# Kernel tuning notes

Measured on AMD Instinct MI355X. Metric: run time of the kernel, lower is better.

## Reference

```python
import jax, jax.numpy as jnp
import numpy as np

N = 10000        # num_nodes
F_IN = 256       # dataset_num_features
H = 128          # hidden_channels
C_OUT = 40       # dataset_num_classes
L = 3            # num_layers
HEADS = 8
DH = H // HEADS  # per-head dim
E = 160000       # num edges (before self loops)
SCALE = 1.0 / float(np.sqrt(DH))


def setup_inputs() -> dict:
    key = jax.random.key(0)
    ks = jax.random.split(key, 8)
    s = lambda k, *sh: (jax.random.normal(k, sh, dtype=jnp.float32) * 0.05)
    return dict(
        edge_index=jax.random.randint(ks[0], (2, E), 0, N, dtype=jnp.int32),
        x_param=s(ks[1], N, F_IN),
        lin1_w=s(ks[2], F_IN, H),
        lin1_b=jnp.zeros((H,), jnp.float32),
        wq=s(ks[3], L, H, H),
        wk=s(ks[4], L, H, H),
        wv=s(ks[5], L, H, H),
        bq=jnp.zeros((L, H), jnp.float32),
        bk=jnp.zeros((L, H), jnp.float32),
        bv=jnp.zeros((L, H), jnp.float32),
        lin2_w=s(ks[6], H, C_OUT),
        lin2_b=jnp.zeros((C_OUT,), jnp.float32),
    )


def _gcn_norm(edge_index):
    # PyG gcn_norm: add self loops (weight 1), symmetric D^-1/2 A D^-1/2
    loops = jnp.arange(N, dtype=edge_index.dtype)
    row = jnp.concatenate([edge_index[0], loops])  # source j
    col = jnp.concatenate([edge_index[1], loops])  # target i
    deg = jax.ops.segment_sum(jnp.ones(row.shape, jnp.float32), col, num_segments=N)
    dis = jnp.where(deg > 0, jax.lax.rsqrt(jnp.maximum(deg, 1e-12)), 0.0)
    return row, col, dis[row] * dis[col]


def _restricted_softmax(score):
    # softmax with an implicit extra logit at `margin=0`
    m = jnp.maximum(jnp.max(score, axis=-1, keepdims=True), 0.0)
    e = jnp.exp(score - m)
    return e / (jnp.sum(e, axis=-1, keepdims=True) + jnp.exp(-m))


def _forward(edge_index, x_param, lin1_w, lin1_b, wq, wk, wv, bq, bk, bv, lin2_w, lin2_b):
    row, col, norm = _gcn_norm(edge_index)
    # dropouts are eval-mode no-ops
    x = jax.nn.relu(x_param @ lin1_w + lin1_b)  # [N, H]
    x_all = x[:, None, :]                       # [N, 1, H]
    for l in range(L):
        t = x_all.shape[1]
        # project per-node first (linear commutes with per-edge gather)
        q = (x_all[:, -1] @ wq[l] + bq[l]).reshape(N, HEADS, DH)      # query from latest state
        k = (x_all @ wk[l] + bk[l]).reshape(N, t, HEADS, DH)          # keys over full history
        v = (x_all @ wv[l] + bv[l]).reshape(N, t, HEADS, DH)
        qe = q[col]   # [Etot, heads, dh]   (x_i)
        ke = k[row]   # [Etot, t, heads, dh] (x_j)
        ve = v[row]
        score = jnp.einsum('ehd,ethd->eht', qe, ke) * SCALE
        attn = _restricted_softmax(score)        # attention-dropout is a no-op in eval
        msg = jnp.einsum('eht,ethd->ehd', attn, ve).reshape(-1, H) * norm[:, None]
        out = jax.ops.segment_sum(msg, col, num_segments=N)  # aggr='add'
        x = jax.nn.relu(out)
        x_all = jnp.concatenate([x_all, x[:, None, :]], axis=1)
    logits = x_all[:, -1] @ lin2_w + lin2_b
    return jax.nn.log_softmax(logits, axis=1)


def reference(edge_index, x_param, lin1_w, lin1_b, wq, wk, wv, bq, bk, bv, lin2_w, lin2_b):
    return _forward(edge_index, x_param, lin1_w, lin1_b, wq, wk, wv, bq, bk, bv, lin2_w, lin2_b)
```

## Files before the change

### kernel.cpp

```cpp
#include <hip/hip_runtime.h>
#include <math.h>

#define N_NODES 10000
#define F_IN_D  256
#define H_DIM   128
#define C_OUTD  40
#define NHEADS  8
#define NEDGES  160000
#define ETOT    (NEDGES + N_NODES)
#define SCALE_F 0.25f
#define TILES_N 157

typedef __attribute__((ext_vector_type(8))) short bf16x8;
typedef __attribute__((ext_vector_type(4))) float f32x4;
typedef __attribute__((ext_vector_type(2))) float f32x2;

__device__ __forceinline__ unsigned short f2bf(float f) {
    unsigned int u = __float_as_uint(f);
    unsigned int r = (u + 0x7FFFu + ((u >> 16) & 1u)) >> 16;
    return (unsigned short)r;
}
__device__ __forceinline__ float bf2f(unsigned short h) {
    return __uint_as_float(((unsigned int)h) << 16);
}
__device__ __forceinline__ unsigned char f2fp8(float v) {
    int pk = __builtin_amdgcn_cvt_pk_fp8_f32(v, v, 0, false);
    return (unsigned char)(pk & 0xff);
}


__global__ void k_deg_count(const int* __restrict__ col, int* degi) {
    int e = blockIdx.x * 256 + threadIdx.x;
    if (e < NEDGES) atomicAdd(&degi[col[e]], 1);
}

__global__ void k_scan(const int* __restrict__ degi, int* offsets, int* cursor) {
    __shared__ int part[256];
    int tid = threadIdx.x;
    int s = 0;
    if (tid < 250) {
        const int4* d4 = (const int4*)degi;
        for (int i = 0; i < 10; ++i) {
            int4 v = d4[tid * 10 + i];
            s += v.x + v.y + v.z + v.w;
        }
    }
    part[tid] = s;
    __syncthreads();
    for (int off = 1; off < 256; off <<= 1) {
        int v = 0;
        if (tid >= off) v = part[tid - off];
        __syncthreads();
        part[tid] += v;
        __syncthreads();
    }
    if (tid < 250) {
        int base = part[tid] - s;
        int beg = tid * 40;
        for (int i = 0; i < 40; ++i) {
            offsets[beg + i] = base;
            cursor[beg + i]  = 0;
            base += degi[beg + i];
        }
    }
}

__global__ void k_scatter(const int* __restrict__ row, const int* __restrict__ col,
                          const int* __restrict__ degi, const int* __restrict__ offsets,
                          int* cursor, int* csr_row, float* csr_norm) {
    int e = blockIdx.x * 256 + threadIdx.x;
    if (e >= ETOT) return;
    int r, c;
    if (e < NEDGES) { r = row[e]; c = col[e]; }
    else            { r = c = e - NEDGES; }
    int slot = offsets[c] + atomicAdd(&cursor[c], 1);
    float dr = rsqrtf((float)degi[r]);
    float dc = rsqrtf((float)degi[c]);
    csr_row[slot]  = r;
    csr_norm[slot] = dr * dc;
}


__global__ void k_prep(const float* __restrict__ w1, const float* __restrict__ wq,
                       const float* __restrict__ wk, const float* __restrict__ wv,
                       const float* __restrict__ w2,
                       unsigned short* __restrict__ W1T, unsigned short* __restrict__ WTq,
                       unsigned short* __restrict__ WTk, unsigned short* __restrict__ WTv,
                       unsigned short* __restrict__ W2T, int* __restrict__ degi) {
    int b = blockIdx.x;
    if (b < 728) {
        int e = b * 256 + threadIdx.x;
        if (e < 32768) {
            int n = e >> 8, k = e & 255;
            W1T[e] = f2bf(w1[k * H_DIM + n]);
        } else if (e < 180224) {
            int e2 = e - 32768;
            int mat = e2 >> 14;
            int r   = e2 & 16383;
            int n = r >> 7, k = r & 127;
            int l = mat / 3, ws = mat % 3;
            const float*    src = (ws == 0) ? wq  : (ws == 1) ? wk  : wv;
            unsigned short* dst = (ws == 0) ? WTq : (ws == 1) ? WTk : WTv;
            dst[l * 16384 + n * H_DIM + k] = f2bf(src[l * 16384 + k * H_DIM + n]);
        } else if (e < 186368) {
            int e3 = e - 180224;
            int c = e3 >> 7, k = e3 & 127;
            W2T[c * H_DIM + k] = (c < C_OUTD) ? f2bf(w2[k * C_OUTD + c]) : 0;
        }
    } else {
        int i = (b - 728) * 256 + threadIdx.x;
        if (i < N_NODES) degi[i] = 1;
    }
}


__global__ __launch_bounds__(256) void k_lin1_mfma(const float* __restrict__ X,
                                                   const unsigned short* __restrict__ W1T,
                                                   const float* __restrict__ b1,
                                                   unsigned short* __restrict__ X0,
                                                   int nct) {
    int tid = threadIdx.x;
    int wid = tid >> 6, lane = tid & 63;
    int m = lane & 15, quad = lane >> 4;
    int rowA = blockIdx.x * 64 + wid * 16 + m;
    int rowc = rowA < N_NODES ? rowA : N_NODES - 1;
    bf16x8 af[8];
    const float* ap = X + (size_t)rowc * F_IN_D + quad * 8;
    #pragma unroll
    for (int s = 0; s < 8; ++s) {
        float4 lo = *(const float4*)(ap + s * 32);
        float4 hi = *(const float4*)(ap + s * 32 + 4);
        union { unsigned short u[8]; bf16x8 v; } pk;
        pk.u[0] = f2bf(lo.x); pk.u[1] = f2bf(lo.y);
        pk.u[2] = f2bf(lo.z); pk.u[3] = f2bf(lo.w);
        pk.u[4] = f2bf(hi.x); pk.u[5] = f2bf(hi.y);
        pk.u[6] = f2bf(hi.z); pk.u[7] = f2bf(hi.w);
        af[s] = pk.v;
    }
    int row0 = blockIdx.x * 64 + wid * 16 + quad * 4;
    for (int ct = 0; ct < nct; ++ct) {
        int col = ct * 16 + m;
        const unsigned short* bp = W1T + (size_t)col * F_IN_D + quad * 8;
        f32x4 acc = {0.f, 0.f, 0.f, 0.f};
        #pragma unroll
        for (int s = 0; s < 8; ++s) {
            bf16x8 bfr = __builtin_bit_cast(bf16x8, *(const uint4*)(bp + s * 32));
            acc = __builtin_amdgcn_mfma_f32_16x16x32_bf16(af[s], bfr, acc, 0, 0, 0);
        }
        float bb = b1[col];
        #pragma unroll
        for (int rg = 0; rg < 4; ++rg) {
            int r = row0 + rg;
            if (r < N_NODES)
                X0[(size_t)r * H_DIM + col] = f2bf(fmaxf(acc[rg] + bb, 0.f));
        }
    }
}


__global__ __launch_bounds__(256) void k_qkv_mfma(const unsigned short* __restrict__ XHb,
                                                  const unsigned short* __restrict__ WTq,
                                                  const unsigned short* __restrict__ WTk,
                                                  const unsigned short* __restrict__ WTv,
                                                  const float* __restrict__ bq,
                                                  const float* __restrict__ bk,
                                                  const float* __restrict__ bv,
                                                  unsigned short* __restrict__ Qb,
                                                  unsigned char* __restrict__ KVb,
                                                  int l, int t, int nct) {
    int tid = threadIdx.x;
    int wid = tid >> 6, lane = tid & 63;
    int m = lane & 15, quad = lane >> 4;
    int mi = blockIdx.x / TILES_N;
    int rt = blockIdx.x % TILES_N;
    const unsigned short* WT; const float* bias; int slice, mode;
    if (mi == 0)      { WT = WTq; bias = bq; slice = l;          mode = 0; }
    else if (mi <= t) { WT = WTk; bias = bk; slice = mi - 1;     mode = 1; }
    else              { WT = WTv; bias = bv; slice = mi - t - 1; mode = 2; }
    const unsigned short* A = XHb + (size_t)slice * N_NODES * H_DIM;
    int rowA = rt * 64 + wid * 16 + m;
    bf16x8 af[4];
    const unsigned short* ap = A + (size_t)rowA * H_DIM + quad * 8;
    #pragma unroll
    for (int s = 0; s < 4; ++s)
        af[s] = __builtin_bit_cast(bf16x8, *(const uint4*)(ap + s * 32));
    int row0 = rt * 64 + wid * 16 + quad * 4;
    int vofs = (mode == 2) ? 8 : 0;
    for (int cp = 0; cp < nct; ++cp) {
        int colA = cp * 32 + m;
        int colB = colA + 16;
        const unsigned short* bpA = WT + (size_t)colA * H_DIM + quad * 8;
        const unsigned short* bpB = WT + (size_t)colB * H_DIM + quad * 8;
        bf16x8 bA[4], bB[4];
        #pragma unroll
        for (int s = 0; s < 4; ++s) {
            bA[s] = __builtin_bit_cast(bf16x8, *(const uint4*)(bpA + s * 32));
            bB[s] = __builtin_bit_cast(bf16x8, *(const uint4*)(bpB + s * 32));
        }
        f32x4 accA = {0.f, 0.f, 0.f, 0.f};
        f32x4 accB = {0.f, 0.f, 0.f, 0.f};
        #pragma unroll
        for (int s = 0; s < 4; ++s) {
            accA = __builtin_amdgcn_mfma_f32_16x16x32_bf16(af[s], bA[s], accA, 0, 0, 0);
            accB = __builtin_amdgcn_mfma_f32_16x16x32_bf16(af[s], bB[s], accB, 0, 0, 0);
        }
        float bbA = bias[colA], bbB = bias[colB];
        #pragma unroll
        for (int rg = 0; rg < 4; ++rg) {
            int r = row0 + rg;
            if (r < N_NODES) {
                float vA = accA[rg] + bbA;
                float vB = accB[rg] + bbB;
                if (mode == 0) {
                    Qb[(size_t)r * H_DIM + colA] = f2bf(vA);
                    Qb[(size_t)r * H_DIM + colB] = f2bf(vB);
                } else {
                    size_t nb = ((size_t)r * 3 + slice) * 256;
                    KVb[nb + (colA >> 3) * 16 + (colA & 7) + vofs] = f2fp8(vA);
                    KVb[nb + (colB >> 3) * 16 + (colB & 7) + vofs] = f2fp8(vB);
                }
            }
        }
    }
}


template <int T>
__global__ __launch_bounds__(256) void k_attn_agg(const unsigned short* __restrict__ Q,
                                                  const uint4* __restrict__ KV,
                                                  const int* __restrict__ csr_row,
                                                  const float* __restrict__ csr_norm,
                                                  const int* __restrict__ offsets,
                                                  const int* __restrict__ degi,
                                                  unsigned int* __restrict__ Xout) {
    int tid = threadIdx.x;
    int wid = tid >> 6, lane = tid & 63;
    int quarter = lane >> 4, ci = lane & 15;
    int n = blockIdx.x * 4 + wid;
    float q[8];
    {
        uint4 qp = *(const uint4*)&Q[(size_t)n * H_DIM + ci * 8];
        q[0] = __uint_as_float(qp.x << 16) * SCALE_F;
        q[1] = __uint_as_float(qp.x & 0xffff0000u) * SCALE_F;
        q[2] = __uint_as_float(qp.y << 16) * SCALE_F;
        q[3] = __uint_as_float(qp.y & 0xffff0000u) * SCALE_F;
        q[4] = __uint_as_float(qp.z << 16) * SCALE_F;
        q[5] = __uint_as_float(qp.z & 0xffff0000u) * SCALE_F;
        q[6] = __uint_as_float(qp.w << 16) * SCALE_F;
        q[7] = __uint_as_float(qp.w & 0xffff0000u) * SCALE_F;
    }
    int start = offsets[n];
    int cnt   = degi[n];
    int nq = (cnt + 3) >> 2;
    float a[8];
    #pragma unroll
    for (int i = 0; i < 8; ++i) a[i] = 0.f;

    for (int j = 0; j < nq; ++j) {
        int j4 = j * 4 + quarter;
        int valid = j4 < cnt;
        int idx = start + (valid ? j4 : 0);
        int   r   = csr_row[idx];
        float nrm = valid ? csr_norm[idx] : 0.f;
        const uint4* kvp = KV + (size_t)r * 48 + ci;
        uint4 kv[T];
        #pragma unroll
        for (int s = 0; s < T; ++s) kv[s] = kvp[s * 16];
        float sc[T];
        #pragma unroll
        for (int s = 0; s < T; ++s) {
            f32x2 k0 = __builtin_amdgcn_cvt_pk_f32_fp8(kv[s].x, false);
            f32x2 k1 = __builtin_amdgcn_cvt_pk_f32_fp8(kv[s].x, true);
            f32x2 k2 = __builtin_amdgcn_cvt_pk_f32_fp8(kv[s].y, false);
            f32x2 k3 = __builtin_amdgcn_cvt_pk_f32_fp8(kv[s].y, true);
            float p = q[0] * k0[0] + q[1] * k0[1] + q[2] * k1[0] + q[3] * k1[1]
                    + q[4] * k2[0] + q[5] * k2[1] + q[6] * k3[0] + q[7] * k3[1];
            p += __shfl_xor(p, 1, 2);
            sc[s] = p;
        }
        float m = 0.f;
        #pragma unroll
        for (int s = 0; s < T; ++s) m = fmaxf(m, sc[s]);
        float den = __expf(-m);
        float mv[8];
        #pragma unroll
        for (int i = 0; i < 8; ++i) mv[i] = 0.f;
        #pragma unroll
        for (int s = 0; s < T; ++s) {
            float w = __expf(sc[s] - m);
            den += w;
            f32x2 v0 = __builtin_amdgcn_cvt_pk_f32_fp8(kv[s].z, false);
            f32x2 v1 = __builtin_amdgcn_cvt_pk_f32_fp8(kv[s].z, true);
            f32x2 v2 = __builtin_amdgcn_cvt_pk_f32_fp8(kv[s].w, false);
            f32x2 v3 = __builtin_amdgcn_cvt_pk_f32_fp8(kv[s].w, true);
            mv[0] += w * v0[0]; mv[1] += w * v0[1];
            mv[2] += w * v1[0]; mv[3] += w * v1[1];
            mv[4] += w * v2[0]; mv[5] += w * v2[1];
            mv[6] += w * v3[0]; mv[7] += w * v3[1];
        }
        float ws = __fdividef(nrm, den);
        #pragma unroll
        for (int i = 0; i < 8; ++i) a[i] += ws * mv[i];
    }
    #pragma unroll
    for (int i = 0; i < 8; ++i) {
        a[i] += __shfl_xor(a[i], 16, 64);
        a[i] += __shfl_xor(a[i], 32, 64);
    }
    if (quarter == 0) {
        uint4 o;
        o.x = ((unsigned int)f2bf(fmaxf(a[1], 0.f)) << 16) | (unsigned int)f2bf(fmaxf(a[0], 0.f));
        o.y = ((unsigned int)f2bf(fmaxf(a[3], 0.f)) << 16) | (unsigned int)f2bf(fmaxf(a[2], 0.f));
        o.z = ((unsigned int)f2bf(fmaxf(a[5], 0.f)) << 16) | (unsigned int)f2bf(fmaxf(a[4], 0.f));
        o.w = ((unsigned int)f2bf(fmaxf(a[7], 0.f)) << 16) | (unsigned int)f2bf(fmaxf(a[6], 0.f));
        *(uint4*)&Xout[(size_t)n * 64 + ci * 4] = o;
    }
}


__global__ __launch_bounds__(256) void k_lin2_mfma(const unsigned short* __restrict__ X,
                                                   const unsigned short* __restrict__ W2T,
                                                   const float* __restrict__ b2,
                                                   float* __restrict__ out) {
    int tid = threadIdx.x;
    int wid = tid >> 6, lane = tid & 63;
    int m = lane & 15, quad = lane >> 4;
    int rowA = blockIdx.x * 64 + wid * 16 + m;
    bf16x8 af[4];
    const unsigned short* ap = X + (size_t)rowA * H_DIM + quad * 8;
    #pragma unroll
    for (int s = 0; s < 4; ++s)
        af[s] = __builtin_bit_cast(bf16x8, *(const uint4*)(ap + s * 32));

    f32x4 acc0 = {0.f, 0.f, 0.f, 0.f};
    f32x4 acc1 = {0.f, 0.f, 0.f, 0.f};
    f32x4 acc2 = {0.f, 0.f, 0.f, 0.f};
    const unsigned short* bp0 = W2T + (size_t)(m)      * H_DIM + quad * 8;
    const unsigned short* bp1 = W2T + (size_t)(16 + m) * H_DIM + quad * 8;
    const unsigned short* bp2 = W2T + (size_t)(32 + m) * H_DIM + quad * 8;
    #pragma unroll
    for (int s = 0; s < 4; ++s) {
        bf16x8 b0 = __builtin_bit_cast(bf16x8, *(const uint4*)(bp0 + s * 32));
        acc0 = __builtin_amdgcn_mfma_f32_16x16x32_bf16(af[s], b0, acc0, 0, 0, 0);
        bf16x8 b1 = __builtin_bit_cast(bf16x8, *(const uint4*)(bp1 + s * 32));
        acc1 = __builtin_amdgcn_mfma_f32_16x16x32_bf16(af[s], b1, acc1, 0, 0, 0);
        bf16x8 b2f = __builtin_bit_cast(bf16x8, *(const uint4*)(bp2 + s * 32));
        acc2 = __builtin_amdgcn_mfma_f32_16x16x32_bf16(af[s], b2f, acc2, 0, 0, 0);
    }

    float bb0 = b2[m], bb1 = b2[16 + m];
    float bb2 = (m < 8) ? b2[32 + m] : 0.f;
    int row0 = blockIdx.x * 64 + wid * 16 + quad * 4;
    #pragma unroll
    for (int rg = 0; rg < 4; ++rg) {
        int r = row0 + rg;
        float v0 = acc0[rg] + bb0;
        float v1 = acc1[rg] + bb1;
        float v2 = (m < 8) ? (acc2[rg] + bb2) : -INFINITY;
        float mx = fmaxf(fmaxf(v0, v1), v2);
        #pragma unroll
        for (int o = 8; o > 0; o >>= 1) mx = fmaxf(mx, __shfl_xor(mx, o, 16));
        float sm = __expf(v0 - mx) + __expf(v1 - mx) + ((m < 8) ? __expf(v2 - mx) : 0.f);
        #pragma unroll
        for (int o = 8; o > 0; o >>= 1) sm += __shfl_xor(sm, o, 16);
        float lse = mx + __logf(sm);
        if (r < N_NODES) {
            out[(size_t)r * C_OUTD + m]      = v0 - lse;
            out[(size_t)r * C_OUTD + 16 + m] = v1 - lse;
            if (m < 8) out[(size_t)r * C_OUTD + 32 + m] = v2 - lse;
        }
    }
}


extern "C" void kernel_launch(void* const* d_in, const int* in_sizes, int n_in,
                              void* d_out, int out_size, void* d_ws, size_t ws_size,
                              hipStream_t stream) {
    const int*   ei      = (const int*)d_in[0];
    const int*   row     = ei;
    const int*   col     = ei + NEDGES;
    const float* x_param = (const float*)d_in[1];
    const float* lin1_w  = (const float*)d_in[2];
    const float* lin1_b  = (const float*)d_in[3];
    const float* wq      = (const float*)d_in[4];
    const float* wk      = (const float*)d_in[5];
    const float* wv      = (const float*)d_in[6];
    const float* bq      = (const float*)d_in[7];
    const float* bk      = (const float*)d_in[8];
    const float* bv      = (const float*)d_in[9];
    const float* lin2_w  = (const float*)d_in[10];
    const float* lin2_b  = (const float*)d_in[11];
    float*       out     = (float*)d_out;

    char* wbase = (char*)d_ws;
    size_t off = 0;
    auto alloc = [&](size_t bytes) -> void* {
        off = (off + 255) & ~(size_t)255;
        void* p = wbase + off;
        off += bytes;
        return p;
    };
    int*            degi     = (int*)           alloc((size_t)N_NODES * 4);
    int*            offsets  = (int*)           alloc((size_t)N_NODES * 4);
    int*            cursor   = (int*)           alloc((size_t)N_NODES * 4);
    int*            csr_row  = (int*)           alloc((size_t)ETOT * 4);
    float*          csr_norm = (float*)         alloc((size_t)ETOT * 4);
    unsigned short* W1T      = (unsigned short*)alloc((size_t)H_DIM * F_IN_D * 2);
    unsigned short* WTq      = (unsigned short*)alloc((size_t)3 * H_DIM * H_DIM * 2);
    unsigned short* WTk      = (unsigned short*)alloc((size_t)3 * H_DIM * H_DIM * 2);
    unsigned short* WTv      = (unsigned short*)alloc((size_t)3 * H_DIM * H_DIM * 2);
    unsigned short* W2T      = (unsigned short*)alloc((size_t)48 * H_DIM * 2);
    unsigned short* XHb      = (unsigned short*)alloc((size_t)4 * N_NODES * H_DIM * 2);
    unsigned short* Qb       = (unsigned short*)alloc((size_t)N_NODES * H_DIM * 2);
    unsigned char*  KVb      = (unsigned char*) alloc((size_t)N_NODES * 3 * 256);

    k_prep<<<768, 256, 0, stream>>>(lin1_w, wq, wk, wv, lin2_w,
                                    W1T, WTq, WTk, WTv, W2T, degi);
    k_deg_count<<<(NEDGES + 255) / 256, 256, 0, stream>>>(col, degi);
    k_scan     <<<1, 256, 0, stream>>>(degi, offsets, cursor);
    k_scatter  <<<(ETOT + 255) / 256, 256, 0, stream>>>(row, col, degi, offsets, cursor,
                                                        csr_row, csr_norm);

    k_lin1_mfma<<<TILES_N, 256, 0, stream>>>(x_param, W1T, lin1_b, XHb, 8);

    for (int l = 0; l < 3; ++l) {
        int t = l + 1;
        k_qkv_mfma<<<(1 + 2 * t) * TILES_N, 256, 0, stream>>>(
            XHb, WTq + (size_t)l * 16384, WTk + (size_t)l * 16384, WTv + (size_t)l * 16384,
            bq + l * H_DIM, bk + l * H_DIM, bv + l * H_DIM,
            Qb, KVb, l, t, 4);
        unsigned int* Xnext = (unsigned int*)(XHb + (size_t)(l + 1) * N_NODES * H_DIM);
        if (t == 1)
            k_attn_agg<1><<<2500, 256, 0, stream>>>(Qb, (const uint4*)KVb, csr_row,
                                                    csr_norm, offsets, degi, Xnext);
        else if (t == 2)
            k_attn_agg<2><<<2500, 256, 0, stream>>>(Qb, (const uint4*)KVb, csr_row,
                                                    csr_norm, offsets, degi, Xnext);
        else
            k_attn_agg<3><<<2500, 256, 0, stream>>>(Qb, (const uint4*)KVb, csr_row,
                                                    csr_norm, offsets, degi, Xnext);
    }

    k_lin2_mfma<<<TILES_N, 256, 0, stream>>>(XHb + (size_t)3 * N_NODES * H_DIM,
                                             W2T, lin2_b, out);
}
```

Before: 258.7 us.

## Software-pipeline KV gathers in attention and fuse degree counting into prep

The attention-aggregation loop now double-buffers the KV gather: the next neighbor's row index is loaded two steps ahead and its KV vectors one step ahead, so their latency overlaps the current edge's softmax math. Separately, the degree-count kernel is folded into the weight-prep kernel's extra blocks, degree and cursor arrays are zeroed with one memset, and the scan kernel adds the self-loop count and runs with 1024 threads. This removes a kernel launch and hides gather latency, at the cost of more registers in the attention kernel and an extra memset node.

```diff
diff --git a/kernel.cpp b/kernel.cpp
--- a/kernel.cpp
+++ b/kernel.cpp
@@ -29,38 +29,33 @@
 }
 
 
-__global__ void k_deg_count(const int* __restrict__ col, int* degi) {
-    int e = blockIdx.x * 256 + threadIdx.x;
-    if (e < NEDGES) atomicAdd(&degi[col[e]], 1);
-}
-
-__global__ void k_scan(const int* __restrict__ degi, int* offsets, int* cursor) {
-    __shared__ int part[256];
+__global__ void k_scan(int* __restrict__ degi, int* __restrict__ offsets) {
+    __shared__ int part[1024];
     int tid = threadIdx.x;
     int s = 0;
-    if (tid < 250) {
-        const int4* d4 = (const int4*)degi;
-        for (int i = 0; i < 10; ++i) {
-            int4 v = d4[tid * 10 + i];
-            s += v.x + v.y + v.z + v.w;
-        }
+    if (tid < 1000) {
+        int beg = tid * 10;
+        #pragma unroll
+        for (int i = 0; i < 10; ++i) s += degi[beg + i] + 1;
     }
     part[tid] = s;
     __syncthreads();
-    for (int off = 1; off < 256; off <<= 1) {
+    for (int off = 1; off < 1024; off <<= 1) {
         int v = 0;
         if (tid >= off) v = part[tid - off];
         __syncthreads();
         part[tid] += v;
         __syncthreads();
     }
-    if (tid < 250) {
+    if (tid < 1000) {
         int base = part[tid] - s;
-        int beg = tid * 40;
-        for (int i = 0; i < 40; ++i) {
+        int beg = tid * 10;
+        #pragma unroll
+        for (int i = 0; i < 10; ++i) {
+            int d = degi[beg + i] + 1;
             offsets[beg + i] = base;
-            cursor[beg + i]  = 0;
-            base += degi[beg + i];
+            degi[beg + i]    = d;
+            base += d;
         }
     }
 }
@@ -83,7 +78,7 @@
 
 __global__ void k_prep(const float* __restrict__ w1, const float* __restrict__ wq,
                        const float* __restrict__ wk, const float* __restrict__ wv,
-                       const float* __restrict__ w2,
+                       const float* __restrict__ w2, const int* __restrict__ col,
                        unsigned short* __restrict__ W1T, unsigned short* __restrict__ WTq,
                        unsigned short* __restrict__ WTk, unsigned short* __restrict__ WTv,
                        unsigned short* __restrict__ W2T, int* __restrict__ degi) {
@@ -108,8 +103,8 @@
             W2T[c * H_DIM + k] = (c < C_OUTD) ? f2bf(w2[k * C_OUTD + c]) : 0;
         }
     } else {
-        int i = (b - 728) * 256 + threadIdx.x;
-        if (i < N_NODES) degi[i] = 1;
+        int e = (b - 728) * 256 + threadIdx.x;
+        if (e < NEDGES) atomicAdd(&degi[col[e]], 1);
     }
 }
 
@@ -226,6 +221,54 @@
 
 
 template <int T>
+__device__ __forceinline__ void kv_load(const uint4* __restrict__ KV, int r, int ci,
+                                        uint4 (&kv)[T]) {
+    const uint4* p = KV + (size_t)r * 48 + ci;
+    #pragma unroll
+    for (int s = 0; s < T; ++s) kv[s] = p[s * 16];
+}
+
+template <int T>
+__device__ __forceinline__ void edge_accum(const uint4 (&kv)[T], const float (&q)[8],
+                                           float nrm, float (&a)[8]) {
+    float sc[T];
+    #pragma unroll
+    for (int s = 0; s < T; ++s) {
+        f32x2 k0 = __builtin_amdgcn_cvt_pk_f32_fp8(kv[s].x, false);
+        f32x2 k1 = __builtin_amdgcn_cvt_pk_f32_fp8(kv[s].x, true);
+        f32x2 k2 = __builtin_amdgcn_cvt_pk_f32_fp8(kv[s].y, false);
+        f32x2 k3 = __builtin_amdgcn_cvt_pk_f32_fp8(kv[s].y, true);
+        float p = q[0] * k0[0] + q[1] * k0[1] + q[2] * k1[0] + q[3] * k1[1]
+                + q[4] * k2[0] + q[5] * k2[1] + q[6] * k3[0] + q[7] * k3[1];
+        p += __shfl_xor(p, 1, 2);
+        sc[s] = p;
+    }
+    float m = 0.f;
+    #pragma unroll
+    for (int s = 0; s < T; ++s) m = fmaxf(m, sc[s]);
+    float den = __expf(-m);
+    float mv[8];
+    #pragma unroll
+    for (int i = 0; i < 8; ++i) mv[i] = 0.f;
+    #pragma unroll
+    for (int s = 0; s < T; ++s) {
+        float w = __expf(sc[s] - m);
+        den += w;
+        f32x2 v0 = __builtin_amdgcn_cvt_pk_f32_fp8(kv[s].z, false);
+        f32x2 v1 = __builtin_amdgcn_cvt_pk_f32_fp8(kv[s].z, true);
+        f32x2 v2 = __builtin_amdgcn_cvt_pk_f32_fp8(kv[s].w, false);
+        f32x2 v3 = __builtin_amdgcn_cvt_pk_f32_fp8(kv[s].w, true);
+        mv[0] += w * v0[0]; mv[1] += w * v0[1];
+        mv[2] += w * v1[0]; mv[3] += w * v1[1];
+        mv[4] += w * v2[0]; mv[5] += w * v2[1];
+        mv[6] += w * v3[0]; mv[7] += w * v3[1];
+    }
+    float ws = __fdividef(nrm, den);
+    #pragma unroll
+    for (int i = 0; i < 8; ++i) a[i] += ws * mv[i];
+}
+
+template <int T>
 __global__ __launch_bounds__(256) void k_attn_agg(const unsigned short* __restrict__ Q,
                                                   const uint4* __restrict__ KV,
                                                   const int* __restrict__ csr_row,
@@ -256,52 +299,37 @@
     #pragma unroll
     for (int i = 0; i < 8; ++i) a[i] = 0.f;
 
-    for (int j = 0; j < nq; ++j) {
+    auto rowload = [&](int j, int& r, float& nrm) {
         int j4 = j * 4 + quarter;
         int valid = j4 < cnt;
         int idx = start + (valid ? j4 : 0);
-        int   r   = csr_row[idx];
-        float nrm = valid ? csr_norm[idx] : 0.f;
-        const uint4* kvp = KV + (size_t)r * 48 + ci;
-        uint4 kv[T];
-        #pragma unroll
-        for (int s = 0; s < T; ++s) kv[s] = kvp[s * 16];
-        float sc[T];
-        #pragma unroll
-        for (int s = 0; s < T; ++s) {
-            f32x2 k0 = __builtin_amdgcn_cvt_pk_f32_fp8(kv[s].x, false);
-            f32x2 k1 = __builtin_amdgcn_cvt_pk_f32_fp8(kv[s].x, true);
-            f32x2 k2 = __builtin_amdgcn_cvt_pk_f32_fp8(kv[s].y, false);
-            f32x2 k3 = __builtin_amdgcn_cvt_pk_f32_fp8(kv[s].y, true);
-            float p = q[0] * k0[0] + q[1] * k0[1] + q[2] * k1[0] + q[3] * k1[1]
-                    + q[4] * k2[0] + q[5] * k2[1] + q[6] * k3[0] + q[7] * k3[1];
-            p += __shfl_xor(p, 1, 2);
-            sc[s] = p;
-        }
-        float m = 0.f;
-        #pragma unroll
-        for (int s = 0; s < T; ++s) m = fmaxf(m, sc[s]);
-        float den = __expf(-m);
-        float mv[8];
-        #pragma unroll
-        for (int i = 0; i < 8; ++i) mv[i] = 0.f;
-        #pragma unroll
-        for (int s = 0; s < T; ++s) {
-            float w = __expf(sc[s] - m);
-            den += w;
-            f32x2 v0 = __builtin_amdgcn_cvt_pk_f32_fp8(kv[s].z, false);
-            f32x2 v1 = __builtin_amdgcn_cvt_pk_f32_fp8(kv[s].z, true);
-            f32x2 v2 = __builtin_amdgcn_cvt_pk_f32_fp8(kv[s].w, false);
-            f32x2 v3 = __builtin_amdgcn_cvt_pk_f32_fp8(kv[s].w, true);
-            mv[0] += w * v0[0]; mv[1] += w * v0[1];
-            mv[2] += w * v1[0]; mv[3] += w * v1[1];
-            mv[4] += w * v2[0]; mv[5] += w * v2[1];
-            mv[6] += w * v3[0]; mv[7] += w * v3[1];
-        }
-        float ws = __fdividef(nrm, den);
-        #pragma unroll
-        for (int i = 0; i < 8; ++i) a[i] += ws * mv[i];
-    }
+        r = csr_row[idx];
+        nrm = valid ? csr_norm[idx] : 0.f;
+    };
+
+    int r0; float nCUR; rowload(0, r0, nCUR);
+    int rN; float nN;   rowload(1, rN, nN);
+    uint4 kvA[T], kvB[T];
+    kv_load<T>(KV, r0, ci, kvA);
+
+    int j = 0;
+    for (;;) {
+        {
+            int r2; float n2; rowload(j + 2, r2, n2);
+            kv_load<T>(KV, rN, ci, kvB);
+            edge_accum<T>(kvA, q, nCUR, a);
+            nCUR = nN; rN = r2; nN = n2;
+        }
+        if (++j >= nq) break;
+        {
+            int r2; float n2; rowload(j + 2, r2, n2);
+            kv_load<T>(KV, rN, ci, kvA);
+            edge_accum<T>(kvB, q, nCUR, a);
+            nCUR = nN; rN = r2; nN = n2;
+        }
+        if (++j >= nq) break;
+    }
+
     #pragma unroll
     for (int i = 0; i < 8; ++i) {
         a[i] += __shfl_xor(a[i], 16, 64);
@@ -401,8 +429,8 @@
         return p;
     };
     int*            degi     = (int*)           alloc((size_t)N_NODES * 4);
+    int*            cursor   = (int*)           alloc((size_t)N_NODES * 4);
     int*            offsets  = (int*)           alloc((size_t)N_NODES * 4);
-    int*            cursor   = (int*)           alloc((size_t)N_NODES * 4);
     int*            csr_row  = (int*)           alloc((size_t)ETOT * 4);
     float*          csr_norm = (float*)         alloc((size_t)ETOT * 4);
     unsigned short* W1T      = (unsigned short*)alloc((size_t)H_DIM * F_IN_D * 2);
@@ -414,12 +442,13 @@
     unsigned short* Qb       = (unsigned short*)alloc((size_t)N_NODES * H_DIM * 2);
     unsigned char*  KVb      = (unsigned char*) alloc((size_t)N_NODES * 3 * 256);
 
-    k_prep<<<768, 256, 0, stream>>>(lin1_w, wq, wk, wv, lin2_w,
-                                    W1T, WTq, WTk, WTv, W2T, degi);
-    k_deg_count<<<(NEDGES + 255) / 256, 256, 0, stream>>>(col, degi);
-    k_scan     <<<1, 256, 0, stream>>>(degi, offsets, cursor);
-    k_scatter  <<<(ETOT + 255) / 256, 256, 0, stream>>>(row, col, degi, offsets, cursor,
-                                                        csr_row, csr_norm);
+    hipMemsetAsync(degi, 0,
+                   (size_t)((char*)(cursor + N_NODES) - (char*)degi), stream);
+    k_prep<<<1353, 256, 0, stream>>>(lin1_w, wq, wk, wv, lin2_w, col,
+                                     W1T, WTq, WTk, WTv, W2T, degi);
+    k_scan   <<<1, 1024, 0, stream>>>(degi, offsets);
+    k_scatter<<<(ETOT + 255) / 256, 256, 0, stream>>>(row, col, degi, offsets, cursor,
+                                                      csr_row, csr_norm);
 
     k_lin1_mfma<<<TILES_N, 256, 0, stream>>>(x_param, W1T, lin1_b, XHb, 8);
 
```

Result: faster. 247.2 us (-4.5%).
